# Kernel tuning notes

Measured on AMD Instinct MI355X. Metric: run time of the kernel, lower is better.

The kernel has to match this reference:

```python
import jax, jax.numpy as jnp
import numpy as np

B, L, C = 128, 512, 321
PRED = 336
S = 4
K = 25  # moving_avg kernel
EPS = 1e-5
N = L // S          # 128
H = 2048 // S       # 512


def setup_inputs() -> dict:
    key = jax.random.key(0)
    ks = jax.random.split(key, 16)
    def w(k, shape, fan_in):
        return jax.random.uniform(k, shape, jnp.float32, -1.0, 1.0) / np.sqrt(fan_in)
    return {
        "x": jax.random.normal(ks[0], (B, L, C), jnp.float32),
        "revin_w": jnp.ones((C,), jnp.float32),
        "revin_b": jnp.zeros((C,), jnp.float32),
        "W11": w(ks[1], (N, H), N), "b11": w(ks[2], (H,), N),
        "W12": w(ks[3], (H, N), H), "b12": w(ks[4], (N,), H),
        "W21": w(ks[5], (N, H), N), "b21": w(ks[6], (H,), N),
        "W22": w(ks[7], (H, N), H), "b22": w(ks[8], (N,), H),
        "W_tr": w(ks[9], (L, PRED), L), "b_tr": w(ks[10], (PRED,), L),
        "W_se": w(ks[11], (L, PRED), L), "b_se": w(ks[12], (PRED,), L),
    }


def reference(x, revin_w, revin_b, W11, b11, W12, b12, W21, b21, W22, b22,
              W_tr, b_tr, W_se, b_se):
    # RevIN norm (statistics are detached in the original)
    mean = jax.lax.stop_gradient(jnp.mean(x, axis=1, keepdims=True))
    std = jax.lax.stop_gradient(
        jnp.sqrt(jnp.var(x, axis=1, keepdims=True) + EPS))
    xn = (x - mean) / std * revin_w + revin_b  # [B, L, C]

    # Decomp: replicate-pad along time then moving average of width K
    front = jnp.repeat(xn[:, 0:1, :], K - 1 - (K - 1) // 2, axis=1)
    end = jnp.repeat(xn[:, -1:, :], (K - 1) // 2, axis=1)
    padded = jnp.concatenate([front, xn, end], axis=1)  # [B, L+K-1, C]
    cs = jnp.concatenate(
        [jnp.zeros((B, 1, C), padded.dtype), jnp.cumsum(padded, axis=1)], axis=1)
    trend = (cs[:, K:, :] - cs[:, :-K, :]) / K  # [B, L, C]
    seasonal = xn - trend

    trend_p = jnp.transpose(trend, (0, 2, 1))      # [B, C, L]
    seasonal_p = jnp.transpose(seasonal, (0, 2, 1))  # [B, C, L]

    # Trend head: Linear L -> PRED
    trend_out = jnp.einsum('bcl,lp->bcp', trend_p, W_tr) + b_tr

    # Seasonal head: Splitting (strided interleave) = reshape + transpose
    xs = seasonal_p.reshape(B, C, N, S).transpose(0, 1, 3, 2)  # [B, C, S, N]
    h = jnp.matmul(jax.nn.gelu(jnp.matmul(xs, W11) + b11, approximate=False), W12) + b12
    h = jnp.matmul(jax.nn.gelu(jnp.matmul(h, W21) + b21, approximate=False), W22) + b22
    # Catting is the exact inverse interleave
    sea = h.transpose(0, 1, 3, 2).reshape(B, C, L)  # [B, C, L]
    sea_out = jnp.einsum('bcl,lp->bcp', sea, W_se) + b_se

    out = jnp.transpose(trend_out + sea_out, (0, 2, 1))  # [B, PRED, C]

    # RevIN denorm
    out = (out - revin_b) / (revin_w + EPS * EPS)
    out = out * std + mean
    return out
```

## Files before the change

kernel.cpp:

```cpp
#include <hip/hip_runtime.h>
#include <math.h>

#define BB   128
#define LL   512
#define CC   321
#define PREDD 336

using bf16x8  = __attribute__((ext_vector_type(8))) __bf16;
using floatx4 = __attribute__((ext_vector_type(4))) float;
using uintx4  = __attribute__((ext_vector_type(4))) unsigned int;
typedef unsigned short u16;
typedef unsigned int u32;

#define MFMA16(a,b,c) __builtin_amdgcn_mfma_f32_16x16x32_bf16(a,b,c,0,0,0)

__device__ __forceinline__ u16 f2bf(float f){
    union { float f; unsigned u; } v; v.f = f;
    unsigned r = v.u + 0x7FFFu + ((v.u >> 16) & 1u);
    return (u16)(r >> 16);
}

__device__ __forceinline__ u32 cvtpk(float a, float b){
    u32 r;
    asm("v_cvt_pk_bf16_f32 %0, %1, %2" : "=v"(r) : "v"(a), "v"(b));
    return r;
}

__device__ __forceinline__ float fgelu(float x){
    float u = x*(0.7978845608f + 0.035677408f*x*x);
    float a = fminf(u*2.8853900818f, 80.f);
    float t = __builtin_amdgcn_exp2f(a);
    return x*t*__builtin_amdgcn_rcpf(1.f + t);
}

__device__ __forceinline__ int swz128(int r, int s){ return r*128 + (((s & 8) | ((s ^ r) & 7)) << 3); }
__device__ __forceinline__ int swz64 (int r, int s){ return r*64  + (((s ^ r) & 7) << 3); }

__device__ __forceinline__ void dma16(const u16* g, const u16* l){
    __builtin_amdgcn_global_load_lds(
        (const __attribute__((address_space(1))) u32*)g,
        (__attribute__((address_space(3))) u32*)l, 16, 0, 0);
}

__global__ void prep_k(const float* __restrict__ W11, const float* __restrict__ W12,
                       const float* __restrict__ W21, const float* __restrict__ W22,
                       const float* __restrict__ Wtr, const float* __restrict__ Wse,
                       u16* __restrict__ BT1, u16* __restrict__ BT2,
                       u16* __restrict__ BT3, u16* __restrict__ BT4,
                       u16* __restrict__ BT5)
{
    int idx = blockIdx.x * 256 + threadIdx.x;
    if (idx < 65536){
        int h = idx >> 7;
        int k = idx & 127;
        int hp = (h & ~31) | (((h >> 2) & 3)*8 + ((h >> 4) & 1)*4 + (h & 3));
        BT1[idx] = f2bf(W11[k*512 + hp]);
        BT3[idx] = f2bf(W21[k*512 + hp]);
        int n = idx >> 9, k2 = idx & 511;
        int np = ((n >> 5) & 3)*32 + ((n >> 2) & 3)*8 + ((n >> 4) & 1)*4 + (n & 3);
        BT2[idx] = f2bf(W12[k2*128 + np]);
        BT4[idx] = f2bf(W22[k2*128 + n]);
    }
    if (idx < 393216){
        int p = idx >> 10, k = idx & 1023;
        float v = 0.f;
        if (p < PREDD){
            if (k < 512) v = Wtr[k*PREDD + p];
            else { int kk = k - 512; int s = kk >> 7; int n = kk & 127; v = Wse[(4*n + s)*PREDD + p]; }
        }
        BT5[idx] = f2bf(v);
    }
}

#define XT(t,c) xt[((t)<<4) + (((t)>>5)<<1) + (c)]
__global__ __launch_bounds__(256) void decomp_k(
    const float* __restrict__ x, const float* __restrict__ rw, const float* __restrict__ rb,
    u16* __restrict__ Afin, u16* __restrict__ xs, float2* __restrict__ stats)
{
    __shared__ float xt[8240];
    __shared__ float red[2][16][16];
    __shared__ float sh_m[16], sh_istd[16];
    int b = blockIdx.x / 21, ct = blockIdx.x % 21;
    int tid = threadIdx.x;

    int cl = tid & 15, lp = tid >> 4;
    int c = ct*16 + cl;
    bool valid = c < CC;
    const float* xb = x + (size_t)b*LL*CC;
    float s = 0.f, q = 0.f;
    for (int i = 0; i < 32; ++i){
        int t = lp + 16*i;
        float v = valid ? xb[(size_t)t*CC + c] : 0.f;
        XT(t, cl) = v;
        s += v; q += v*v;
    }
    red[0][lp][cl] = s; red[1][lp][cl] = q;
    __syncthreads();
    if (tid < 16){
        float ss = 0.f, qq = 0.f;
        for (int j = 0; j < 16; ++j){ ss += red[0][j][tid]; qq += red[1][j][tid]; }
        float m  = ss * (1.f/512.f);
        float var = qq * (1.f/512.f) - m*m;
        float sd = sqrtf(var + 1e-5f);
        sh_m[tid] = m; sh_istd[tid] = 1.f/sd;
        int cc = ct*16 + tid;
        if (cc < CC) stats[(size_t)b*CC + cc] = make_float2(m, sd);
    }
    __syncthreads();

    int ch = tid >> 4, tp = tid & 15;
    int c2 = ct*16 + ch;
    if (c2 >= CC) return;
    float m = sh_m[ch], istd = sh_istd[ch];
    float w = rw[c2] * istd, bbv = rb[c2];
    size_t bc = (size_t)b*CC + c2;
    u16* tr  = Afin + bc*1024;
    u16* xsr = xs   + bc*512;
    int t0 = tp*32;

    float win = 0.f;
#pragma unroll
    for (int d = -12; d <= 12; ++d){
        int u = t0 + d; u = u < 0 ? 0 : (u > 511 ? 511 : u);
        win += XT(u, ch);
    }
    u16 trbuf[8];
    u16 xsbuf[4][8];
#pragma unroll
    for (int i = 0; i < 32; ++i){
        int t = t0 + i;
        float Ax = win * (1.f/25.f);
        float xv = XT(t, ch);
        trbuf[i & 7] = f2bf((Ax - m)*w + bbv);
        xsbuf[i & 3][i >> 2] = f2bf((xv - Ax)*w);
        if ((i & 7) == 7)
            *(uintx4*)(tr + t0 + (i & ~7)) = *(const uintx4*)trbuf;
        int uo = t - 12; uo = uo < 0 ? 0 : uo;
        int un = t + 13; un = un > 511 ? 511 : un;
        win += XT(un, ch) - XT(uo, ch);
    }
#pragma unroll
    for (int s4 = 0; s4 < 4; ++s4)
        *(uintx4*)(xsr + s4*128 + tp*8) = *(const uintx4*)xsbuf[s4];
}

__global__ __launch_bounds__(256, 3) void mlp_fused_k(
    const u16* __restrict__ xs,
    const u16* __restrict__ BT1, const float* __restrict__ b11,
    const u16* __restrict__ BT2, const float* __restrict__ b12,
    const u16* __restrict__ BT3, const float* __restrict__ b21,
    const u16* __restrict__ BT4, const float* __restrict__ b22,
    u16* __restrict__ Afin)
{
    __shared__ u16 lds[16384];
    const int tid  = threadIdx.x;
    const int lane = tid & 63;
    const int wv   = tid >> 6;
    const int quad = lane >> 4, cl = lane & 15;
    const int wrow = blockIdx.x * 128 + wv * 32;

    const int qq0 = tid, qq1 = tid + 256;
    const int rA0 = qq0 >> 4, spA0 = qq0 & 15;
    const int rA1 = qq1 >> 4, spA1 = qq1 & 15;
    const int offA0 = rA0*128 + (((spA0 & 8) | ((spA0 ^ rA0) & 7)) << 3);
    const int offA1 = rA1*128 + (((spA1 & 8) | ((spA1 ^ rA1) & 7)) << 3);
    const int rB0 = qq0 >> 2, spB0 = qq0 & 3;
    const int rB1 = qq1 >> 2, spB1 = qq1 & 3;
    const int offB0 = rB0*512 + ((spB0 ^ ((rB0 >> 1) & 3)) << 3);
    const int offB1 = rB1*512 + ((spB1 ^ ((rB1 >> 1) & 3)) << 3);

#define STAGE(dst, w1, w2, hcc)                                          \
    dma16((w1) + (hcc)*4096 + offA0, lds + (dst) + qq0*8);               \
    dma16((w1) + (hcc)*4096 + offA1, lds + (dst) + qq1*8);               \
    dma16((w2) + (hcc)*32  + offB0, lds + (dst) + 4096 + qq0*8);         \
    dma16((w2) + (hcc)*32  + offB1, lds + (dst) + 4096 + qq1*8);

    STAGE(0, BT1, BT2, 0)

    bf16x8 xfrag[2][4];
#pragma unroll
    for (int mt = 0; mt < 2; ++mt)
#pragma unroll
        for (int ks = 0; ks < 4; ++ks)
            xfrag[mt][ks] = *(const bf16x8*)(xs + (size_t)(wrow + mt*16 + cl)*128 + ks*32 + quad*8);

    floatx4 Yacc[16];
#pragma unroll
    for (int i = 0; i < 16; ++i) Yacc[i] = (floatx4){0.f,0.f,0.f,0.f};

    __syncthreads();

    const int w2rd = (quad ^ ((cl >> 1) & 3)) << 3;

    for (int g = 0; g < 32; ++g){
        const int cur = (g & 1) ? 8192 : 0;
        if (g < 31){
            const int nxt = 8192 - cur;
            const u16* w1s = ((g+1) & 16) ? BT3 : BT1;
            const u16* w2s = ((g+1) & 16) ? BT4 : BT2;
            const int hn = (g+1) & 15;
            STAGE(nxt, w1s, w2s, hn)
        }
        const float* ba = (g & 16) ? b21 : b11;
        const int hc = g & 15;

        floatx4 hacc[2][2];
        hacc[0][0] = hacc[0][1] = hacc[1][0] = hacc[1][1] = (floatx4){0.f,0.f,0.f,0.f};
#pragma unroll
        for (int ks = 0; ks < 4; ++ks){
            const int sg = ks*4 + quad;
            const int s0 = ((sg & 8) | ((sg ^ cl) & 7)) << 3;
            bf16x8 wf0 = *(const bf16x8*)(lds + cur + cl*128 + s0);
            bf16x8 wf1 = *(const bf16x8*)(lds + cur + (16 + cl)*128 + s0);
#pragma unroll
            for (int mt = 0; mt < 2; ++mt){
                hacc[0][mt] = MFMA16(wf0, xfrag[mt][ks], hacc[0][mt]);
                hacc[1][mt] = MFMA16(wf1, xfrag[mt][ks], hacc[1][mt]);
            }
        }

        const float4 bA = *(const float4*)(ba + hc*32 + quad*8);
        const float4 bB = *(const float4*)(ba + hc*32 + quad*8 + 4);
        bf16x8 a2[2];
#pragma unroll
        for (int mt = 0; mt < 2; ++mt){
            union { bf16x8 v; u32 w[4]; } u;
            u.w[0] = cvtpk(fgelu(hacc[0][mt][0] + bA.x), fgelu(hacc[0][mt][1] + bA.y));
            u.w[1] = cvtpk(fgelu(hacc[0][mt][2] + bA.z), fgelu(hacc[0][mt][3] + bA.w));
            u.w[2] = cvtpk(fgelu(hacc[1][mt][0] + bB.x), fgelu(hacc[1][mt][1] + bB.y));
            u.w[3] = cvtpk(fgelu(hacc[1][mt][2] + bB.z), fgelu(hacc[1][mt][3] + bB.w));
            a2[mt] = u.v;
        }

#pragma unroll
        for (int nt2 = 0; nt2 < 8; ++nt2){
            bf16x8 b2 = *(const bf16x8*)(lds + cur + 4096 + (nt2*16 + cl)*32 + w2rd);
#pragma unroll
            for (int mt = 0; mt < 2; ++mt)
                Yacc[mt*8 + nt2] = MFMA16(b2, a2[mt], Yacc[mt*8 + nt2]);
        }
        __syncthreads();

        if (g == 15){
#pragma unroll
            for (int ks = 0; ks < 4; ++ks){
                const float4 cA = *(const float4*)(b12 + ks*32 + quad*8);
                const float4 cB = *(const float4*)(b12 + ks*32 + quad*8 + 4);
#pragma unroll
                for (int mt = 0; mt < 2; ++mt){
                    floatx4 y0 = Yacc[mt*8 + 2*ks];
                    floatx4 y1 = Yacc[mt*8 + 2*ks + 1];
                    union { bf16x8 v; u32 w[4]; } u;
                    u.w[0] = cvtpk(y0[0] + cA.x, y0[1] + cA.y);
                    u.w[1] = cvtpk(y0[2] + cA.z, y0[3] + cA.w);
                    u.w[2] = cvtpk(y1[0] + cB.x, y1[1] + cB.y);
                    u.w[3] = cvtpk(y1[2] + cB.z, y1[3] + cB.w);
                    xfrag[mt][ks] = u.v;
                }
            }
#pragma unroll
            for (int i = 0; i < 16; ++i) Yacc[i] = (floatx4){0.f,0.f,0.f,0.f};
        }
    }

#pragma unroll
    for (int mt = 0; mt < 2; ++mt){
        const int gr = wrow + mt*16 + cl;
        u16* dst = Afin + (size_t)(gr >> 2)*1024 + 512 + (size_t)(gr & 3)*128 + quad*4;
#pragma unroll
        for (int nt2 = 0; nt2 < 8; ++nt2){
            const float4 cB = *(const float4*)(b22 + nt2*16 + quad*4);
            floatx4 v = Yacc[mt*8 + nt2];
            union { unsigned long long d; u32 w[2]; } u;
            u.w[0] = cvtpk(v[0] + cB.x, v[1] + cB.y);
            u.w[1] = cvtpk(v[2] + cB.z, v[3] + cB.w);
            *(unsigned long long*)(dst + nt2*16) = u.d;
        }
    }
#undef STAGE
}

__global__ __launch_bounds__(256, 2) void head_gemm_k(
    const u16* __restrict__ A, const u16* __restrict__ BT,
    float* __restrict__ Cf,
    const float* __restrict__ bias, const float* __restrict__ bias2,
    const float* __restrict__ rw, const float* __restrict__ rb,
    const float2* __restrict__ stats)
{
    __shared__ u16 lds[32768];
    const int id = blockIdx.x;
    const int xcd = id & 7, slot = id >> 3;
    const int g8 = slot / 3, j = slot - g8*3;
    const int by = xcd + 8*g8;
    if (by >= 321) return;
    const int row0 = by * 128, col0 = j * 128;

    const int tid = threadIdx.x;
    const int lane = tid & 63;
    const int wv = tid >> 6;
    const int wm = wv & 1, wn = wv >> 1;
    const int quad = lane >> 4, cl = lane & 15;

    const int qbase = wv*4*64 + lane;

#pragma unroll
    for (int i = 0; i < 4; ++i){
        int qq = qbase + i*64;
        int r = qq >> 3, p = qq & 7; int s = (p ^ r) & 7;
        dma16(A  + (size_t)(row0 + r)*1024 + s*8, lds + qq*8);
        dma16(BT + (size_t)(col0 + r)*1024 + s*8, lds + 16384 + qq*8);
    }
    __syncthreads();

    floatx4 acc[16];
#pragma unroll
    for (int i = 0; i < 16; ++i) acc[i] = (floatx4){0.f,0.f,0.f,0.f};

    for (int it = 0; it < 16; ++it){
        const int cur = (it & 1) * 8192;
        if (it < 15){
            const int nxt = ((it+1) & 1) * 8192;
            const int k0 = (it+1) * 64;
#pragma unroll
            for (int i = 0; i < 4; ++i){
                int qq = qbase + i*64;
                int r = qq >> 3, p = qq & 7; int s = (p ^ r) & 7;
                dma16(A  + (size_t)(row0 + r)*1024 + k0 + s*8, lds + nxt + qq*8);
                dma16(BT + (size_t)(col0 + r)*1024 + k0 + s*8, lds + 16384 + nxt + qq*8);
            }
        }
#pragma unroll
        for (int kk = 0; kk < 2; ++kk){
            bf16x8 af[4], bfr[4];
#pragma unroll
            for (int mt = 0; mt < 4; ++mt) af[mt]  = *(const bf16x8*)(lds + cur + swz64(wm*64 + mt*16 + cl, kk*4 + quad));
#pragma unroll
            for (int nt = 0; nt < 4; ++nt) bfr[nt] = *(const bf16x8*)(lds + 16384 + cur + swz64(wn*64 + nt*16 + cl, kk*4 + quad));
#pragma unroll
            for (int mt = 0; mt < 4; ++mt)
#pragma unroll
                for (int nt = 0; nt < 4; ++nt)
                    acc[mt*4+nt] = MFMA16(af[mt], bfr[nt], acc[mt*4+nt]);
        }
        __syncthreads();
    }

#pragma unroll
    for (int mt = 0; mt < 4; ++mt)
#pragma unroll
        for (int nt = 0; nt < 4; ++nt){
            floatx4 v = acc[mt*4+nt];
            int gc = col0 + wn*64 + nt*16 + cl;
            if (gc >= PREDD) continue;
            float bsum = bias[gc] + bias2[gc];
#pragma unroll
            for (int i = 0; i < 4; ++i){
                int gr = row0 + wm*64 + mt*16 + quad*4 + i;
                float val = v[i] + bsum;
                int bv2 = gr / CC;
                int c  = gr - bv2*CC;
                val = (val - rb[c]) / (rw[c] + 1e-10f);
                float2 st = stats[gr];
                val = val*st.y + st.x;
                Cf[(size_t)bv2*(PREDD*CC) + (size_t)gc*CC + c] = val;
            }
        }
}

extern "C" void kernel_launch(void* const* d_in, const int* in_sizes, int n_in,
                              void* d_out, int out_size, void* d_ws, size_t ws_size,
                              hipStream_t stream)
{
    const float* x   = (const float*)d_in[0];
    const float* rvw = (const float*)d_in[1];
    const float* rvb = (const float*)d_in[2];
    const float* W11 = (const float*)d_in[3];
    const float* b11 = (const float*)d_in[4];
    const float* W12 = (const float*)d_in[5];
    const float* b12 = (const float*)d_in[6];
    const float* W21 = (const float*)d_in[7];
    const float* b21 = (const float*)d_in[8];
    const float* W22 = (const float*)d_in[9];
    const float* b22 = (const float*)d_in[10];
    const float* Wtr = (const float*)d_in[11];
    const float* btr = (const float*)d_in[12];
    const float* Wse = (const float*)d_in[13];
    const float* bse = (const float*)d_in[14];
    float* out = (float*)d_out;

    char* ws = (char*)d_ws;
    u16* BT1 = (u16*)(ws + 0);
    u16* BT2 = (u16*)(ws + 131072);
    u16* BT3 = (u16*)(ws + 262144);
    u16* BT4 = (u16*)(ws + 393216);
    u16* BT5 = (u16*)(ws + 524288);
    float2* stats = (float2*)(ws + 1310720);
    u16* Afin = (u16*)(ws + 1639424);
    u16* xs   = (u16*)(ws + 85787648);

    hipLaunchKernelGGL(prep_k, dim3(1536), dim3(256), 0, stream,
                       W11, W12, W21, W22, Wtr, Wse, BT1, BT2, BT3, BT4, BT5);
    hipLaunchKernelGGL(decomp_k, dim3(128*21), dim3(256), 0, stream,
                       x, rvw, rvb, Afin, xs, stats);
    hipLaunchKernelGGL(mlp_fused_k, dim3(1284), dim3(256), 0, stream,
                       xs, BT1, b11, BT2, b12, BT3, b21, BT4, b22, Afin);
    hipLaunchKernelGGL(head_gemm_k, dim3(984), dim3(256), 0, stream,
                       Afin, BT5, out, btr, bse, rvw, rvb, stats);
}
```

Baseline: 432.9 us.

## Load MLP weights directly from global in fragment order, dropping LDS staging

prep_k now writes the MLP weight matrices into a per-lane MFMA fragment order, so each wave can read its weight fragments straight from global memory (L2-resident) with contiguous 16-byte loads. This removes the LDS double buffering, the DMA staging and the per-chunk __syncthreads in the fused MLP kernel. Biases are folded into the accumulator initial values, and the GELU reciprocals are batched four at a time to cut rcp instructions. The cost is that every wave issues its own global weight loads, giving more L2 traffic and exposed load latency with no block-level sharing.

```diff
diff --git a/kernel.cpp b/kernel.cpp
--- a/kernel.cpp
+++ b/kernel.cpp
@@ -26,14 +26,6 @@
     return r;
 }
 
-__device__ __forceinline__ float fgelu(float x){
-    float u = x*(0.7978845608f + 0.035677408f*x*x);
-    float a = fminf(u*2.8853900818f, 80.f);
-    float t = __builtin_amdgcn_exp2f(a);
-    return x*t*__builtin_amdgcn_rcpf(1.f + t);
-}
-
-__device__ __forceinline__ int swz128(int r, int s){ return r*128 + (((s & 8) | ((s ^ r) & 7)) << 3); }
 __device__ __forceinline__ int swz64 (int r, int s){ return r*64  + (((s ^ r) & 7) << 3); }
 
 __device__ __forceinline__ void dma16(const u16* g, const u16* l){
@@ -45,21 +37,24 @@
 __global__ void prep_k(const float* __restrict__ W11, const float* __restrict__ W12,
                        const float* __restrict__ W21, const float* __restrict__ W22,
                        const float* __restrict__ Wtr, const float* __restrict__ Wse,
-                       u16* __restrict__ BT1, u16* __restrict__ BT2,
-                       u16* __restrict__ BT3, u16* __restrict__ BT4,
+                       u16* __restrict__ W1all, u16* __restrict__ W2all,
                        u16* __restrict__ BT5)
 {
     int idx = blockIdx.x * 256 + threadIdx.x;
     if (idx < 65536){
-        int h = idx >> 7;
-        int k = idx & 127;
+        int h = idx >> 7, k = idx & 127;
         int hp = (h & ~31) | (((h >> 2) & 3)*8 + ((h >> 4) & 1)*4 + (h & 3));
-        BT1[idx] = f2bf(W11[k*512 + hp]);
-        BT3[idx] = f2bf(W21[k*512 + hp]);
+        int d1 = (h >> 5)*4096 + ((k >> 5)*2 + ((h >> 4) & 1))*512
+               + (((k >> 3) & 3)*16 + (h & 15))*8 + (k & 7);
+        W1all[d1]         = f2bf(W11[k*512 + hp]);
+        W1all[65536 + d1] = f2bf(W21[k*512 + hp]);
+
         int n = idx >> 9, k2 = idx & 511;
         int np = ((n >> 5) & 3)*32 + ((n >> 2) & 3)*8 + ((n >> 4) & 1)*4 + (n & 3);
-        BT2[idx] = f2bf(W12[k2*128 + np]);
-        BT4[idx] = f2bf(W22[k2*128 + n]);
+        int d2 = (k2 >> 5)*4096 + (n >> 4)*512
+               + (((k2 >> 3) & 3)*16 + (n & 15))*8 + (k2 & 7);
+        W2all[d2]         = f2bf(W12[k2*128 + np]);
+        W2all[65536 + d2] = f2bf(W22[k2*128 + n]);
     }
     if (idx < 393216){
         int p = idx >> 10, k = idx & 1023;
@@ -146,36 +141,16 @@
 
 __global__ __launch_bounds__(256, 3) void mlp_fused_k(
     const u16* __restrict__ xs,
-    const u16* __restrict__ BT1, const float* __restrict__ b11,
-    const u16* __restrict__ BT2, const float* __restrict__ b12,
-    const u16* __restrict__ BT3, const float* __restrict__ b21,
-    const u16* __restrict__ BT4, const float* __restrict__ b22,
+    const u16* __restrict__ W1all, const float* __restrict__ b11,
+    const u16* __restrict__ W2all, const float* __restrict__ b12,
+    const float* __restrict__ b21, const float* __restrict__ b22,
     u16* __restrict__ Afin)
 {
-    __shared__ u16 lds[16384];
     const int tid  = threadIdx.x;
     const int lane = tid & 63;
     const int wv   = tid >> 6;
     const int quad = lane >> 4, cl = lane & 15;
-    const int wrow = blockIdx.x * 128 + wv * 32;
-
-    const int qq0 = tid, qq1 = tid + 256;
-    const int rA0 = qq0 >> 4, spA0 = qq0 & 15;
-    const int rA1 = qq1 >> 4, spA1 = qq1 & 15;
-    const int offA0 = rA0*128 + (((spA0 & 8) | ((spA0 ^ rA0) & 7)) << 3);
-    const int offA1 = rA1*128 + (((spA1 & 8) | ((spA1 ^ rA1) & 7)) << 3);
-    const int rB0 = qq0 >> 2, spB0 = qq0 & 3;
-    const int rB1 = qq1 >> 2, spB1 = qq1 & 3;
-    const int offB0 = rB0*512 + ((spB0 ^ ((rB0 >> 1) & 3)) << 3);
-    const int offB1 = rB1*512 + ((spB1 ^ ((rB1 >> 1) & 3)) << 3);
-
-#define STAGE(dst, w1, w2, hcc)                                          \
-    dma16((w1) + (hcc)*4096 + offA0, lds + (dst) + qq0*8);               \
-    dma16((w1) + (hcc)*4096 + offA1, lds + (dst) + qq1*8);               \
-    dma16((w2) + (hcc)*32  + offB0, lds + (dst) + 4096 + qq0*8);         \
-    dma16((w2) + (hcc)*32  + offB1, lds + (dst) + 4096 + qq1*8);
-
-    STAGE(0, BT1, BT2, 0)
+    const int wrow = blockIdx.x * 128 + wv*32;
 
     bf16x8 xfrag[2][4];
 #pragma unroll
@@ -186,82 +161,104 @@
 
     floatx4 Yacc[16];
 #pragma unroll
-    for (int i = 0; i < 16; ++i) Yacc[i] = (floatx4){0.f,0.f,0.f,0.f};
-
-    __syncthreads();
-
-    const int w2rd = (quad ^ ((cl >> 1) & 3)) << 3;
-
-    for (int g = 0; g < 32; ++g){
-        const int cur = (g & 1) ? 8192 : 0;
-        if (g < 31){
-            const int nxt = 8192 - cur;
-            const u16* w1s = ((g+1) & 16) ? BT3 : BT1;
-            const u16* w2s = ((g+1) & 16) ? BT4 : BT2;
-            const int hn = (g+1) & 15;
-            STAGE(nxt, w1s, w2s, hn)
-        }
-        const float* ba = (g & 16) ? b21 : b11;
-        const int hc = g & 15;
-
-        floatx4 hacc[2][2];
-        hacc[0][0] = hacc[0][1] = hacc[1][0] = hacc[1][1] = (floatx4){0.f,0.f,0.f,0.f};
-#pragma unroll
-        for (int ks = 0; ks < 4; ++ks){
-            const int sg = ks*4 + quad;
-            const int s0 = ((sg & 8) | ((sg ^ cl) & 7)) << 3;
-            bf16x8 wf0 = *(const bf16x8*)(lds + cur + cl*128 + s0);
-            bf16x8 wf1 = *(const bf16x8*)(lds + cur + (16 + cl)*128 + s0);
-#pragma unroll
-            for (int mt = 0; mt < 2; ++mt){
-                hacc[0][mt] = MFMA16(wf0, xfrag[mt][ks], hacc[0][mt]);
-                hacc[1][mt] = MFMA16(wf1, xfrag[mt][ks], hacc[1][mt]);
-            }
-        }
-
-        const float4 bA = *(const float4*)(ba + hc*32 + quad*8);
-        const float4 bB = *(const float4*)(ba + hc*32 + quad*8 + 4);
-        bf16x8 a2[2];
+    for (int nt2 = 0; nt2 < 8; ++nt2){
+        const float4 bv = *(const float4*)(b12 + (nt2 >> 1)*32 + quad*8 + (nt2 & 1)*4);
+        floatx4 f = {bv.x, bv.y, bv.z, bv.w};
+        Yacc[nt2] = f; Yacc[8 + nt2] = f;
+    }
+
+    const u16* w1p = W1all + lane*8;
+    const u16* w2p = W2all + lane*8;
+
+#define CHUNK(BA, G, W1C, W2C)                                                       \
+    {                                                                                \
+                                                        \
+        floatx4 hacc[2][2];                                                          \
+        {                                                                            \
+            const float4 c0 = *(const float4*)((BA) + (G)*32 + quad*8);              \
+            const float4 c1 = *(const float4*)((BA) + (G)*32 + quad*8 + 4);          \
+            hacc[0][0] = (floatx4){c0.x,c0.y,c0.z,c0.w}; hacc[0][1] = hacc[0][0];    \
+            hacc[1][0] = (floatx4){c1.x,c1.y,c1.z,c1.w}; hacc[1][1] = hacc[1][0];    \
+        }                                                                            \
+                                         \
+        const u16* w1c = (W1C) + (G)*4096;                                           \
+        bf16x8 wf[8];                                                                \
+        _Pragma("unroll")                                                            \
+        for (int q8 = 0; q8 < 8; ++q8) wf[q8] = *(const bf16x8*)(w1c + q8*512);      \
+        _Pragma("unroll")                                                            \
+        for (int ks = 0; ks < 4; ++ks)                                               \
+            _Pragma("unroll")                                                        \
+            for (int mt = 0; mt < 2; ++mt){                                          \
+                hacc[0][mt] = MFMA16(wf[ks*2+0], xfrag[mt][ks], hacc[0][mt]);        \
+                hacc[1][mt] = MFMA16(wf[ks*2+1], xfrag[mt][ks], hacc[1][mt]);        \
+            }                                                                        \
+                                       \
+        bf16x8 a2[2];                                                                \
+        _Pragma("unroll")                                                            \
+        for (int mt = 0; mt < 2; ++mt){                                              \
+            float xv[8], tv[8], av[8], rv[8];                                        \
+            _Pragma("unroll")                                                        \
+            for (int j = 0; j < 8; ++j){                                             \
+                float xx = hacc[j >> 2][mt][j & 3];                                  \
+                float qf = fmaf(xx*xx, 0.10294321f, 2.30220827f);                    \
+                float vf = fminf(xx*qf, 30.f);                                       \
+                float tf = __builtin_amdgcn_exp2f(vf);                               \
+                xv[j] = xx; tv[j] = tf; av[j] = tf + 1.f;                            \
+            }                                                                        \
+            _Pragma("unroll")                                                        \
+            for (int gq = 0; gq < 8; gq += 4){                                       \
+                float d01 = av[gq]*av[gq+1], d23 = av[gq+2]*av[gq+3];                \
+                float inv = __builtin_amdgcn_rcpf(d01*d23);                          \
+                float i01 = inv*d23, i23 = inv*d01;                                  \
+                rv[gq]   = i01*av[gq+1]; rv[gq+1] = i01*av[gq];                      \
+                rv[gq+2] = i23*av[gq+3]; rv[gq+3] = i23*av[gq+2];                    \
+            }                                                                        \
+            union { bf16x8 v; u32 w[4]; } uu;                                        \
+            _Pragma("unroll")                                                        \
+            for (int p = 0; p < 4; ++p)                                              \
+                uu.w[p] = cvtpk(xv[2*p]*tv[2*p]*rv[2*p],                             \
+                                xv[2*p+1]*tv[2*p+1]*rv[2*p+1]);                      \
+            a2[mt] = uu.v;                                                           \
+        }                                                                            \
+                                         \
+        const u16* w2c = (W2C) + (G)*4096;                                           \
+        bf16x8 b2[8];                                                                \
+        _Pragma("unroll")                                                            \
+        for (int nt2 = 0; nt2 < 8; ++nt2) b2[nt2] = *(const bf16x8*)(w2c + nt2*512); \
+        _Pragma("unroll")                                                            \
+        for (int nt2 = 0; nt2 < 8; ++nt2)                                            \
+            _Pragma("unroll")                                                        \
+            for (int mt = 0; mt < 2; ++mt)                                           \
+                Yacc[mt*8 + nt2] = MFMA16(b2[nt2], a2[mt], Yacc[mt*8 + nt2]);        \
+    }
+
+    for (int g = 0; g < 16; ++g)
+        CHUNK(b11, g, w1p, w2p)
+
+#pragma unroll
+    for (int ks = 0; ks < 4; ++ks)
 #pragma unroll
         for (int mt = 0; mt < 2; ++mt){
-            union { bf16x8 v; u32 w[4]; } u;
-            u.w[0] = cvtpk(fgelu(hacc[0][mt][0] + bA.x), fgelu(hacc[0][mt][1] + bA.y));
-            u.w[1] = cvtpk(fgelu(hacc[0][mt][2] + bA.z), fgelu(hacc[0][mt][3] + bA.w));
-            u.w[2] = cvtpk(fgelu(hacc[1][mt][0] + bB.x), fgelu(hacc[1][mt][1] + bB.y));
-            u.w[3] = cvtpk(fgelu(hacc[1][mt][2] + bB.z), fgelu(hacc[1][mt][3] + bB.w));
-            a2[mt] = u.v;
-        }
-
-#pragma unroll
-        for (int nt2 = 0; nt2 < 8; ++nt2){
-            bf16x8 b2 = *(const bf16x8*)(lds + cur + 4096 + (nt2*16 + cl)*32 + w2rd);
-#pragma unroll
-            for (int mt = 0; mt < 2; ++mt)
-                Yacc[mt*8 + nt2] = MFMA16(b2, a2[mt], Yacc[mt*8 + nt2]);
-        }
-        __syncthreads();
-
-        if (g == 15){
-#pragma unroll
-            for (int ks = 0; ks < 4; ++ks){
-                const float4 cA = *(const float4*)(b12 + ks*32 + quad*8);
-                const float4 cB = *(const float4*)(b12 + ks*32 + quad*8 + 4);
-#pragma unroll
-                for (int mt = 0; mt < 2; ++mt){
-                    floatx4 y0 = Yacc[mt*8 + 2*ks];
-                    floatx4 y1 = Yacc[mt*8 + 2*ks + 1];
-                    union { bf16x8 v; u32 w[4]; } u;
-                    u.w[0] = cvtpk(y0[0] + cA.x, y0[1] + cA.y);
-                    u.w[1] = cvtpk(y0[2] + cA.z, y0[3] + cA.w);
-                    u.w[2] = cvtpk(y1[0] + cB.x, y1[1] + cB.y);
-                    u.w[3] = cvtpk(y1[2] + cB.z, y1[3] + cB.w);
-                    xfrag[mt][ks] = u.v;
-                }
-            }
-#pragma unroll
-            for (int i = 0; i < 16; ++i) Yacc[i] = (floatx4){0.f,0.f,0.f,0.f};
-        }
-    }
+            floatx4 y0 = Yacc[mt*8 + 2*ks], y1 = Yacc[mt*8 + 2*ks + 1];
+            union { bf16x8 v; u32 w[4]; } uu;
+            uu.w[0] = cvtpk(y0[0], y0[1]); uu.w[1] = cvtpk(y0[2], y0[3]);
+            uu.w[2] = cvtpk(y1[0], y1[1]); uu.w[3] = cvtpk(y1[2], y1[3]);
+            xfrag[mt][ks] = uu.v;
+        }
+#pragma unroll
+    for (int nt2 = 0; nt2 < 8; ++nt2){
+        const float4 bv = *(const float4*)(b22 + nt2*16 + quad*4);
+        floatx4 f = {bv.x, bv.y, bv.z, bv.w};
+        Yacc[nt2] = f; Yacc[8 + nt2] = f;
+    }
+
+    {
+        const u16* w1q = w1p + 65536;
+        const u16* w2q = w2p + 65536;
+        for (int g = 0; g < 16; ++g)
+            CHUNK(b21, g, w1q, w2q)
+    }
+#undef CHUNK
 
 #pragma unroll
     for (int mt = 0; mt < 2; ++mt){
@@ -269,15 +266,13 @@
         u16* dst = Afin + (size_t)(gr >> 2)*1024 + 512 + (size_t)(gr & 3)*128 + quad*4;
 #pragma unroll
         for (int nt2 = 0; nt2 < 8; ++nt2){
-            const float4 cB = *(const float4*)(b22 + nt2*16 + quad*4);
             floatx4 v = Yacc[mt*8 + nt2];
-            union { unsigned long long d; u32 w[2]; } u;
-            u.w[0] = cvtpk(v[0] + cB.x, v[1] + cB.y);
-            u.w[1] = cvtpk(v[2] + cB.z, v[3] + cB.w);
-            *(unsigned long long*)(dst + nt2*16) = u.d;
-        }
-    }
-#undef STAGE
+            union { unsigned long long d; u32 w[2]; } uu;
+            uu.w[0] = cvtpk(v[0], v[1]);
+            uu.w[1] = cvtpk(v[2], v[3]);
+            *(unsigned long long*)(dst + nt2*16) = uu.d;
+        }
+    }
 }
 
 __global__ __launch_bounds__(256, 2) void head_gemm_k(
@@ -389,21 +384,19 @@
     float* out = (float*)d_out;
 
     char* ws = (char*)d_ws;
-    u16* BT1 = (u16*)(ws + 0);
-    u16* BT2 = (u16*)(ws + 131072);
-    u16* BT3 = (u16*)(ws + 262144);
-    u16* BT4 = (u16*)(ws + 393216);
-    u16* BT5 = (u16*)(ws + 524288);
+    u16* W1all = (u16*)(ws + 0);
+    u16* W2all = (u16*)(ws + 262144);
+    u16* BT5   = (u16*)(ws + 524288);
     float2* stats = (float2*)(ws + 1310720);
     u16* Afin = (u16*)(ws + 1639424);
     u16* xs   = (u16*)(ws + 85787648);
 
     hipLaunchKernelGGL(prep_k, dim3(1536), dim3(256), 0, stream,
-                       W11, W12, W21, W22, Wtr, Wse, BT1, BT2, BT3, BT4, BT5);
+                       W11, W12, W21, W22, Wtr, Wse, W1all, W2all, BT5);
     hipLaunchKernelGGL(decomp_k, dim3(128*21), dim3(256), 0, stream,
                        x, rvw, rvb, Afin, xs, stats);
     hipLaunchKernelGGL(mlp_fused_k, dim3(1284), dim3(256), 0, stream,
-                       xs, BT1, b11, BT2, b12, BT3, b21, BT4, b22, Afin);
+                       xs, W1all, b11, W2all, b12, b21, b22, Afin);
     hipLaunchKernelGGL(head_gemm_k, dim3(984), dim3(256), 0, stream,
                        Afin, BT5, out, btr, bse, rvw, rvb, stats);
 }
```

After: 531.2 us. 1.23x slower.
